# Performance work log

Hardware: AMD Instinct MI355X
Metric: run time of the kernel (lower is better)

The kernel has to match this reference:

```python
import jax, jax.numpy as jnp
import numpy as np

N = 20000      # total nodes (batched graph)
E = 320000     # total edges
G = 200        # number of graphs in batch
F_IN = 128     # node_feat_dim
HID = 128      # hidden_dim
H = 4          # num_heads
LAT = 128      # latent_dim
O1, O2, O3 = HID // 2, HID, 2 * HID          # per-head out feats of gat1/2/3
D1, D2, D3 = H * O1, H * O2, H * O3          # flattened dims (256, 512, 1024)
NEG_SLOPE = 0.2


def setup_inputs() -> dict:
    key = jax.random.key(0)
    ks = jax.random.split(key, 26)
    nrm = lambda k, shape, fan: jax.random.normal(k, shape, jnp.float32) / np.sqrt(fan)
    inp = {
        "node_feat": jax.random.normal(ks[0], (N, F_IN), jnp.float32),
        "src": jax.random.randint(ks[1], (E,), 0, N),
        "dst": jax.random.randint(ks[2], (E,), 0, N),
        "graph_ids": jnp.sort(jax.random.randint(ks[3], (N,), 0, G)),
        # GAT layer 1
        "W1": nrm(ks[4], (F_IN, D1), F_IN), "al1": nrm(ks[5], (H, O1), O1),
        "ar1": nrm(ks[6], (H, O1), O1), "b1": jnp.zeros((D1,), jnp.float32),
        # GAT layer 2
        "W2": nrm(ks[7], (D1, D2), D1), "al2": nrm(ks[8], (H, O2), O2),
        "ar2": nrm(ks[9], (H, O2), O2), "b2": jnp.zeros((D2,), jnp.float32),
        # GAT layer 3
        "W3": nrm(ks[10], (D2, D3), D2), "al3": nrm(ks[11], (H, O3), O3),
        "ar3": nrm(ks[12], (H, O3), O3), "b3": jnp.zeros((D3,), jnp.float32),
        # gate MLP of GlobalAttentionPooling: Linear(D3,HID)->ReLU->Linear(HID,1)
        "Wg1": nrm(ks[13], (D3, HID), D3), "bg1": jnp.zeros((HID,), jnp.float32),
        "Wg2": nrm(ks[14], (HID, 1), HID), "bg2": jnp.zeros((1,), jnp.float32),
        # latent heads
        "Wmu": nrm(ks[15], (D3, LAT), D3), "bmu": jnp.zeros((LAT,), jnp.float32),
        "Wlv": nrm(ks[16], (D3, LAT), D3), "blv": jnp.zeros((LAT,), jnp.float32),
    }
    return inp


def gat_layer(x, W, al, ar, b, src, dst, out_feat):
    # dgl GATConv: fc -> per-node attn halves -> edge leaky_relu -> segment softmax over dst -> scatter-agg
    feat = (x @ W).reshape(-1, H, out_feat)            # [N,H,O]
    el = jnp.sum(feat * al[None], axis=-1)             # [N,H]
    er = jnp.sum(feat * ar[None], axis=-1)             # [N,H]
    e = jax.nn.leaky_relu(el[src] + er[dst], NEG_SLOPE)  # [E,H]
    emax = jax.ops.segment_max(e, dst, num_segments=N)   # per-dst max (stable softmax)
    ex = jnp.exp(e - emax[dst])                         # [E,H]
    denom = jax.ops.segment_sum(ex, dst, num_segments=N)
    alpha = ex / jnp.maximum(denom[dst], 1e-9)          # [E,H]
    msg = feat[src] * alpha[..., None]                  # [E,H,O]
    rst = jax.ops.segment_sum(msg, dst, num_segments=N)  # [N,H,O] (zero for 0-in-degree)
    return rst.reshape(-1, H * out_feat) + b            # flatten(1) + bias


def reference(node_feat, src, dst, graph_ids,
              W1, al1, ar1, b1, W2, al2, ar2, b2, W3, al3, ar3, b3,
              Wg1, bg1, Wg2, bg2, Wmu, bmu, Wlv, blv):
    h = jax.nn.elu(gat_layer(node_feat, W1, al1, ar1, b1, src, dst, O1))
    h = jax.nn.elu(gat_layer(h, W2, al2, ar2, b2, src, dst, O2))
    h = jax.nn.elu(gat_layer(h, W3, al3, ar3, b3, src, dst, O3))
    # GlobalAttentionPooling: gate MLP -> per-graph softmax over nodes -> weighted sum
    gate = (jax.nn.relu(h @ Wg1 + bg1) @ Wg2 + bg2)[:, 0]          # [N]
    gmax = jax.ops.segment_max(gate, graph_ids, num_segments=G)
    gexp = jnp.exp(gate - gmax[graph_ids])
    gsum = jax.ops.segment_sum(gexp, graph_ids, num_segments=G)
    a = gexp / jnp.maximum(gsum[graph_ids], 1e-9)                  # [N]
    graph_emb = jax.ops.segment_sum(a[:, None] * h, graph_ids, num_segments=G)  # [G,D3]
    return graph_emb @ Wmu + bmu, graph_emb @ Wlv + blv
```

## Files before the change

### kernel.cpp

```cpp
#include <hip/hip_runtime.h>
#include <math.h>

constexpr int N_NODES = 20000;
constexpr int N_EDGES = 320000;
constexpr int N_GRAPH = 200;
constexpr int F_IN    = 128;
constexpr int NH      = 4;
constexpr int O1 = 64,  O2 = 128, O3 = 256;
constexpr int D1 = 256, D2 = 512, D3 = 1024;
constexpr int LAT  = 128;
constexpr int HIDG = 128;
constexpr int KS_HEADS = 8;
constexpr float NEG_SLOPE = 0.2f;

typedef __attribute__((ext_vector_type(8))) short bf16x8;
typedef __attribute__((ext_vector_type(4))) float f32x4;
typedef __attribute__((ext_vector_type(2))) ushort ushortx2;

__device__ inline void bsplit(float x, ushort& h, ushort& l) {
    unsigned u = __float_as_uint(x);
    unsigned rh = (u + 0x7fffu + ((u >> 16) & 1u)) & 0xffff0000u;
    h = (ushort)(rh >> 16);
    float res = x - __uint_as_float(rh);
    unsigned u2 = __float_as_uint(res);
    l = (ushort)((u2 + 0x7fffu + ((u2 >> 16) & 1u)) >> 16);
}
__device__ inline ushort f2bf(float x) {
    unsigned u = __float_as_uint(x);
    return (ushort)((u + 0x7fffu + ((u >> 16) & 1u)) >> 16);
}
__device__ inline float bf2f(ushort u) { return __uint_as_float(((unsigned)u) << 16); }

__global__ void zero_int(int* __restrict__ p, int n) {
    int i = blockIdx.x * blockDim.x + threadIdx.x;
    if (i < n) p[i] = 0;
}

__global__ void count_deg(const int* __restrict__ dst, int* __restrict__ deg) {
    int e = blockIdx.x * blockDim.x + threadIdx.x;
    if (e < N_EDGES) atomicAdd(&deg[dst[e]], 1);
}

constexpr int SCAN_B = 512;
__global__ __launch_bounds__(SCAN_B)
void scan1(const int* __restrict__ deg, int* __restrict__ rowptr, int* __restrict__ bsum) {
    __shared__ int s[SCAN_B];
    int tid = threadIdx.x;
    int i = blockIdx.x * SCAN_B + tid;
    int v = (i < N_NODES) ? deg[i] : 0;
    s[tid] = v;
    __syncthreads();
    for (int off = 1; off < SCAN_B; off <<= 1) {
        int add = (tid >= off) ? s[tid - off] : 0;
        __syncthreads();
        s[tid] += add;
        __syncthreads();
    }
    if (i < N_NODES) rowptr[i] = s[tid] - v;
    if (tid == SCAN_B - 1) bsum[blockIdx.x] = s[tid];
}

__global__ void scan2(const int* __restrict__ bsum, int* __restrict__ boff, int nblk) {
    if (threadIdx.x == 0 && blockIdx.x == 0) {
        int run = 0;
        for (int b = 0; b < nblk; ++b) { boff[b] = run; run += bsum[b]; }
    }
}

__global__ __launch_bounds__(SCAN_B)
void scan3(int* __restrict__ rowptr, const int* __restrict__ boff, int* __restrict__ pos) {
    int i = blockIdx.x * SCAN_B + threadIdx.x;
    if (i < N_NODES) {
        int v = rowptr[i] + boff[blockIdx.x];
        rowptr[i] = v;
        pos[i] = v;
    }
    if (i == 0) rowptr[N_NODES] = N_EDGES;
}

__global__ void fill_csr(const int* __restrict__ src, const int* __restrict__ dst,
                         int* __restrict__ pos, int* __restrict__ csr_src) {
    int e = blockIdx.x * blockDim.x + threadIdx.x;
    if (e >= N_EDGES) return;
    int slot = atomicAdd(&pos[dst[e]], 1);
    csr_src[slot] = src[e];
}

__global__ void gptr_kernel(const int* __restrict__ gid, int* __restrict__ gptr) {
    int g = blockIdx.x * blockDim.x + threadIdx.x;
    if (g > N_GRAPH) return;
    int lo = 0, hi = N_NODES;
    while (lo < hi) { int mid = (lo + hi) >> 1; if (gid[mid] < g) lo = mid + 1; else hi = mid; }
    gptr[g] = lo;
}

__global__ void split_x(const float* __restrict__ X, ushort* __restrict__ S, int M, int K) {
    int i = blockIdx.x * 256 + threadIdx.x;
    int total = (M * K) >> 2;
    if (i >= total) return;
    int e0 = i << 2;
    int m = e0 / K, k = e0 % K;
    float4 v = *(const float4*)&X[(size_t)m * K + k];
    ushort h[4], l[4];
    bsplit(v.x, h[0], l[0]); bsplit(v.y, h[1], l[1]);
    bsplit(v.z, h[2], l[2]); bsplit(v.w, h[3], l[3]);
    uint2 hp, lp;
    hp.x = (unsigned)h[0] | ((unsigned)h[1] << 16);
    hp.y = (unsigned)h[2] | ((unsigned)h[3] << 16);
    lp.x = (unsigned)l[0] | ((unsigned)l[1] << 16);
    lp.y = (unsigned)l[2] | ((unsigned)l[3] << 16);
    *(uint2*)&S[(size_t)m * 2 * K + k] = hp;
    *(uint2*)&S[(size_t)m * 2 * K + K + k] = lp;
}

__global__ __launch_bounds__(256)
void split_wt(const float* __restrict__ W, ushort* __restrict__ Bt, int K, int N) {
    __shared__ float t[32][33];
    int n0 = blockIdx.x * 32, k0 = blockIdx.y * 32;
    int tx = threadIdx.x, ty = threadIdx.y;
    for (int j = 0; j < 32; j += 8)
        t[ty + j][tx] = W[(size_t)(k0 + ty + j) * N + n0 + tx];
    __syncthreads();
    for (int j = 0; j < 32; j += 8) {
        float v = t[tx][ty + j];
        int n = n0 + ty + j, k = k0 + tx;
        ushort h, l;
        bsplit(v, h, l);
        Bt[(size_t)n * 2 * K + k] = h;
        Bt[(size_t)n * 2 * K + K + k] = l;
    }
}

#define GLOAD_LDS16(g, s) \
    __builtin_amdgcn_global_load_lds((const __attribute__((address_space(1))) void*)(g), \
                                     (__attribute__((address_space(3))) void*)(s), 16, 0, 0)

template<bool BIAS, bool RELU, int OMODE>
__global__ __launch_bounds__(256)
void gemm_mfma(const ushort* __restrict__ Asp, const ushort* __restrict__ Bt,
               const float* __restrict__ bias, void* __restrict__ Cout,
               int M, int N, int K, int ntn, int kchunk) {
    __shared__ __align__(16) ushort lds[4 * 128 * 64];
    constexpr int AH = 0, AL = 128 * 64, BH = 2 * 128 * 64, BL = 3 * 128 * 64;

    const int nwg = gridDim.x;
    int bid = blockIdx.x;
    int q = nwg >> 3, r = nwg & 7;
    int xcd = bid & 7, local = bid >> 3;
    int wg = (xcd < r) ? (xcd * (q + 1) + local) : (r * (q + 1) + (xcd - r) * q + local);
    const int tm = wg / ntn, tn = wg % ntn;

    const int tid = threadIdx.x;
    const int w = tid >> 6, l = tid & 63;
    const int wr = w >> 1, wc = w & 1;
    const size_t sA = 2 * (size_t)K;

    const int ld8 = l >> 3;
    const int stg_col = ((l & 7) ^ ld8) << 3;
    const int r15 = l & 15, kq = l >> 4;
    const int swz = (l & 7) << 4;

    const int k_begin = blockIdx.y * kchunk;
    const int k_end = (k_begin + kchunk < K) ? (k_begin + kchunk) : K;

    f32x4 acc[4][4];
    #pragma unroll
    for (int m = 0; m < 4; ++m)
        #pragma unroll
        for (int n = 0; n < 4; ++n)
            acc[m][n] = 0.f;

    for (int k0 = k_begin; k0 < k_end; k0 += 64) {
        #pragma unroll
        for (int i = 0; i < 4; ++i) {
            int r0 = w * 32 + i * 8;
            int garow = tm * 128 + r0 + ld8;
            if (garow > M - 1) garow = M - 1;
            const ushort* gaH = Asp + (size_t)garow * sA + k0 + stg_col;
            GLOAD_LDS16(gaH, &lds[AH + r0 * 64]);
            GLOAD_LDS16(gaH + K, &lds[AL + r0 * 64]);
            int gbrow = tn * 128 + r0 + ld8;
            const ushort* gbH = Bt + (size_t)gbrow * sA + k0 + stg_col;
            GLOAD_LDS16(gbH, &lds[BH + r0 * 64]);
            GLOAD_LDS16(gbH + K, &lds[BL + r0 * 64]);
        }
        asm volatile("s_waitcnt vmcnt(0)");
        __syncthreads();

        #pragma unroll
        for (int ks = 0; ks < 2; ++ks) {
            const int kbyte = (ks * 64 + kq * 16) ^ swz;
            bf16x8 ah[4], bh[4], xl[4];
            #pragma unroll
            for (int m = 0; m < 4; ++m) {
                int row = wr * 64 + m * 16 + r15;
                ah[m] = *(const bf16x8*)((const char*)&lds[AH] + row * 128 + kbyte);
            }
            #pragma unroll
            for (int n = 0; n < 4; ++n) {
                int row = wc * 64 + n * 16 + r15;
                bh[n] = *(const bf16x8*)((const char*)&lds[BH] + row * 128 + kbyte);
            }
            #pragma unroll
            for (int m = 0; m < 4; ++m)
                #pragma unroll
                for (int n = 0; n < 4; ++n)
                    acc[m][n] = __builtin_amdgcn_mfma_f32_16x16x32_bf16(ah[m], bh[n], acc[m][n], 0, 0, 0);
            #pragma unroll
            for (int m = 0; m < 4; ++m) {
                int row = wr * 64 + m * 16 + r15;
                xl[m] = *(const bf16x8*)((const char*)&lds[AL] + row * 128 + kbyte);
            }
            #pragma unroll
            for (int m = 0; m < 4; ++m)
                #pragma unroll
                for (int n = 0; n < 4; ++n)
                    acc[m][n] = __builtin_amdgcn_mfma_f32_16x16x32_bf16(xl[m], bh[n], acc[m][n], 0, 0, 0);
            #pragma unroll
            for (int n = 0; n < 4; ++n) {
                int row = wc * 64 + n * 16 + r15;
                xl[n] = *(const bf16x8*)((const char*)&lds[BL] + row * 128 + kbyte);
            }
            #pragma unroll
            for (int m = 0; m < 4; ++m)
                #pragma unroll
                for (int n = 0; n < 4; ++n)
                    acc[m][n] = __builtin_amdgcn_mfma_f32_16x16x32_bf16(ah[m], xl[n], acc[m][n], 0, 0, 0);
        }
        __syncthreads();
    }

    #pragma unroll
    for (int m = 0; m < 4; ++m) {
        #pragma unroll
        for (int n = 0; n < 4; ++n) {
            #pragma unroll
            for (int j = 0; j < 4; ++j) {
                int row = tm * 128 + wr * 64 + m * 16 + kq * 4 + j;
                int col = tn * 128 + wc * 64 + n * 16 + r15;
                if (row < M) {
                    float v = acc[m][n][j];
                    if (BIAS) v += bias[col];
                    if (RELU) v = fmaxf(v, 0.f);
                    if (OMODE == 1)
                        ((ushort*)Cout)[(size_t)row * N + col] = f2bf(v);
                    else if (OMODE == 2)
                        ((float*)Cout)[(size_t)blockIdx.y * M * N + (size_t)row * N + col] = v;
                    else
                        ((float*)Cout)[(size_t)row * N + col] = v;
                }
            }
        }
    }
}

__global__ __launch_bounds__(256)
void attn_lr_b(const ushort* __restrict__ feat, const float* __restrict__ al,
               const float* __restrict__ ar, float* __restrict__ el,
               float* __restrict__ er, int O) {
    int n = blockIdx.x;
    int h = threadIdx.x >> 6;
    int lane = threadIdx.x & 63;
    const ushort* fr = feat + (size_t)n * (NH * O) + h * O;
    const float* alr = al + h * O;
    const float* arr = ar + h * O;
    float sl = 0.f, sr = 0.f;
    for (int o = lane * 2; o < O; o += 128) {
        ushortx2 u = *(const ushortx2*)(fr + o);
        float f0 = bf2f(u[0]), f1 = bf2f(u[1]);
        float2 a2 = *(const float2*)(alr + o);
        float2 r2 = *(const float2*)(arr + o);
        sl += f0 * a2.x + f1 * a2.y;
        sr += f0 * r2.x + f1 * r2.y;
    }
    #pragma unroll
    for (int off = 32; off; off >>= 1) {
        sl += __shfl_down(sl, off);
        sr += __shfl_down(sr, off);
    }
    if (lane == 0) {
        el[n * NH + h] = sl;
        er[n * NH + h] = sr;
    }
}

__global__ __launch_bounds__(64)
void attn_softmax(const float* __restrict__ el, const float* __restrict__ er,
                  const int* __restrict__ rowptr, const int* __restrict__ csr_src,
                  float* __restrict__ csrE, float* __restrict__ rden) {
    int d = blockIdx.x;
    int lane = threadIdx.x;
    int base = __builtin_amdgcn_readfirstlane(rowptr[d]);
    int end  = __builtin_amdgcn_readfirstlane(rowptr[d + 1]);
    float4 erd = *(const float4*)(er + d * NH);

    float mx[NH] = {-INFINITY, -INFINITY, -INFINITY, -INFINITY};
    for (int s = base + lane; s < end; s += 64) {
        int sn = csr_src[s];
        float4 elv = *(const float4*)(el + sn * NH);
        float e0 = elv.x + erd.x, e1 = elv.y + erd.y;
        float e2 = elv.z + erd.z, e3 = elv.w + erd.w;
        e0 = (e0 >= 0.f) ? e0 : NEG_SLOPE * e0;
        e1 = (e1 >= 0.f) ? e1 : NEG_SLOPE * e1;
        e2 = (e2 >= 0.f) ? e2 : NEG_SLOPE * e2;
        e3 = (e3 >= 0.f) ? e3 : NEG_SLOPE * e3;
        csrE[(size_t)0 * N_EDGES + s] = e0;
        csrE[(size_t)1 * N_EDGES + s] = e1;
        csrE[(size_t)2 * N_EDGES + s] = e2;
        csrE[(size_t)3 * N_EDGES + s] = e3;
        mx[0] = fmaxf(mx[0], e0); mx[1] = fmaxf(mx[1], e1);
        mx[2] = fmaxf(mx[2], e2); mx[3] = fmaxf(mx[3], e3);
    }
    #pragma unroll
    for (int h = 0; h < NH; ++h)
        #pragma unroll
        for (int off = 32; off; off >>= 1)
            mx[h] = fmaxf(mx[h], __shfl_xor(mx[h], off));

    float sm[NH] = {0.f, 0.f, 0.f, 0.f};
    for (int s = base + lane; s < end; s += 64) {
        #pragma unroll
        for (int h = 0; h < NH; ++h) {
            float ex = expf(csrE[(size_t)h * N_EDGES + s] - mx[h]);
            csrE[(size_t)h * N_EDGES + s] = ex;
            sm[h] += ex;
        }
    }
    #pragma unroll
    for (int h = 0; h < NH; ++h)
        #pragma unroll
        for (int off = 32; off; off >>= 1)
            sm[h] += __shfl_xor(sm[h], off);

    if (lane == 0) {
        #pragma unroll
        for (int h = 0; h < NH; ++h)
            rden[d * NH + h] = 1.f / fmaxf(sm[h], 1e-9f);
    }
}

template<int OSHIFT, int NCH, int D>
__global__ __launch_bounds__(64)
void aggregate_x(const ushort* __restrict__ feat, const float* __restrict__ csrE,
                 const float* __restrict__ rden, const int* __restrict__ rowptr,
                 const int* __restrict__ csr_src, const float* __restrict__ bias,
                 ushort* __restrict__ Ssp) {
    int bid = blockIdx.x;
    int chunk = bid % NCH;
    int d = bid / NCH;
    int t = threadIdx.x;
    int base = __builtin_amdgcn_readfirstlane(rowptr[d]);
    int end  = __builtin_amdgcn_readfirstlane(rowptr[d + 1]);
    const int col0 = chunk * 128 + t * 2;
    const int h = col0 >> OSHIFT;
    const float* eh = csrE + (size_t)h * N_EDGES;
    const ushort* fcol = feat + col0;

    float acc0 = 0.f, acc1 = 0.f;

    int s = base;
    for (; s < end && (s & 3); ++s) {
        int sn = csr_src[s];
        float a = eh[s];
        ushortx2 u = *(const ushortx2*)(fcol + (size_t)sn * D);
        acc0 += bf2f(u[0]) * a; acc1 += bf2f(u[1]) * a;
    }
    for (; s + 7 < end; s += 8) {
        int4 sa = *(const int4*)(csr_src + s);
        int4 sb = *(const int4*)(csr_src + s + 4);
        float4 aa = *(const float4*)(eh + s);
        float4 ab = *(const float4*)(eh + s + 4);
        ushortx2 u0 = *(const ushortx2*)(fcol + (size_t)sa.x * D);
        ushortx2 u1 = *(const ushortx2*)(fcol + (size_t)sa.y * D);
        ushortx2 u2 = *(const ushortx2*)(fcol + (size_t)sa.z * D);
        ushortx2 u3 = *(const ushortx2*)(fcol + (size_t)sa.w * D);
        ushortx2 u4 = *(const ushortx2*)(fcol + (size_t)sb.x * D);
        ushortx2 u5 = *(const ushortx2*)(fcol + (size_t)sb.y * D);
        ushortx2 u6 = *(const ushortx2*)(fcol + (size_t)sb.z * D);
        ushortx2 u7 = *(const ushortx2*)(fcol + (size_t)sb.w * D);
        acc0 += bf2f(u0[0]) * aa.x; acc1 += bf2f(u0[1]) * aa.x;
        acc0 += bf2f(u1[0]) * aa.y; acc1 += bf2f(u1[1]) * aa.y;
        acc0 += bf2f(u2[0]) * aa.z; acc1 += bf2f(u2[1]) * aa.z;
        acc0 += bf2f(u3[0]) * aa.w; acc1 += bf2f(u3[1]) * aa.w;
        acc0 += bf2f(u4[0]) * ab.x; acc1 += bf2f(u4[1]) * ab.x;
        acc0 += bf2f(u5[0]) * ab.y; acc1 += bf2f(u5[1]) * ab.y;
        acc0 += bf2f(u6[0]) * ab.z; acc1 += bf2f(u6[1]) * ab.z;
        acc0 += bf2f(u7[0]) * ab.w; acc1 += bf2f(u7[1]) * ab.w;
    }
    if (s + 3 < end) {
        int4 sn = *(const int4*)(csr_src + s);
        float4 av = *(const float4*)(eh + s);
        ushortx2 u0 = *(const ushortx2*)(fcol + (size_t)sn.x * D);
        ushortx2 u1 = *(const ushortx2*)(fcol + (size_t)sn.y * D);
        ushortx2 u2 = *(const ushortx2*)(fcol + (size_t)sn.z * D);
        ushortx2 u3 = *(const ushortx2*)(fcol + (size_t)sn.w * D);
        acc0 += bf2f(u0[0]) * av.x; acc1 += bf2f(u0[1]) * av.x;
        acc0 += bf2f(u1[0]) * av.y; acc1 += bf2f(u1[1]) * av.y;
        acc0 += bf2f(u2[0]) * av.z; acc1 += bf2f(u2[1]) * av.z;
        acc0 += bf2f(u3[0]) * av.w; acc1 += bf2f(u3[1]) * av.w;
        s += 4;
    }
    for (; s < end; ++s) {
        int sn = csr_src[s];
        float a = eh[s];
        ushortx2 u = *(const ushortx2*)(fcol + (size_t)sn * D);
        acc0 += bf2f(u[0]) * a; acc1 += bf2f(u[1]) * a;
    }

    float rd = rden[d * NH + h];
    float v0 = acc0 * rd + bias[col0];
    float v1 = acc1 * rd + bias[col0 + 1];
    v0 = (v0 > 0.f) ? v0 : expm1f(v0);
    v1 = (v1 > 0.f) ? v1 : expm1f(v1);
    ushort h0, l0, h1, l1;
    bsplit(v0, h0, l0);
    bsplit(v1, h1, l1);
    ushort* hrow = Ssp + (size_t)d * 2 * D;
    ushortx2 hp, lp;
    hp[0] = h0; hp[1] = h1;
    lp[0] = l0; lp[1] = l1;
    *(ushortx2*)(hrow + col0) = hp;
    *(ushortx2*)(hrow + D + col0) = lp;
}

__global__ __launch_bounds__(128)
void gate_reduce(const float* __restrict__ part, const float* __restrict__ bg1,
                 const float* __restrict__ Wg2, const float* __restrict__ bg2,
                 float* __restrict__ gate) {
    int n = blockIdx.x;
    int t = threadIdx.x;
    constexpr size_t CH = (size_t)N_NODES * HIDG;
    size_t idx = (size_t)n * HIDG + t;
    float v = part[idx] + part[CH + idx] + part[2 * CH + idx] + part[3 * CH + idx] + bg1[t];
    v = fmaxf(v, 0.f) * Wg2[t];
    __shared__ float red[128];
    red[t] = v;
    __syncthreads();
    for (int s = 64; s; s >>= 1) {
        if (t < s) red[t] += red[t + s];
        __syncthreads();
    }
    if (t == 0) gate[n] = red[0] + bg2[0];
}

__global__ __launch_bounds__(64)
void gate_stats(const float* __restrict__ gate, const int* __restrict__ gptr,
                float* __restrict__ anorm) {
    int g = blockIdx.x;
    int lane = threadIdx.x;
    int s = __builtin_amdgcn_readfirstlane(gptr[g]);
    int e = __builtin_amdgcn_readfirstlane(gptr[g + 1]);
    float m = -INFINITY;
    for (int n = s + lane; n < e; n += 64) m = fmaxf(m, gate[n]);
    #pragma unroll
    for (int off = 32; off; off >>= 1) m = fmaxf(m, __shfl_xor(m, off));
    float sum = 0.f;
    for (int n = s + lane; n < e; n += 64) sum += expf(gate[n] - m);
    #pragma unroll
    for (int off = 32; off; off >>= 1) sum += __shfl_xor(sum, off);
    float inv = 1.f / fmaxf(sum, 1e-9f);
    for (int n = s + lane; n < e; n += 64) anorm[n] = expf(gate[n] - m) * inv;
}

__global__ __launch_bounds__(64)
void pool_gather(const ushort* __restrict__ h3sp, const float* __restrict__ anorm,
                 const int* __restrict__ gptr, float* __restrict__ gemb) {
    int g = blockIdx.y;
    int col = blockIdx.x * 128 + threadIdx.x * 2;
    float acc0 = 0.f, acc1 = 0.f;
    int s = __builtin_amdgcn_readfirstlane(gptr[g]);
    int e = __builtin_amdgcn_readfirstlane(gptr[g + 1]);
    int n = s;
    for (; n + 3 < e; n += 4) {
        const ushort* r0 = h3sp + (size_t)(n + 0) * 2 * D3;
        const ushort* r1 = h3sp + (size_t)(n + 1) * 2 * D3;
        const ushort* r2 = h3sp + (size_t)(n + 2) * 2 * D3;
        const ushort* r3 = h3sp + (size_t)(n + 3) * 2 * D3;
        float a0 = anorm[n], a1 = anorm[n + 1], a2 = anorm[n + 2], a3 = anorm[n + 3];
        ushortx2 h0 = *(const ushortx2*)(r0 + col), l0 = *(const ushortx2*)(r0 + D3 + col);
        ushortx2 h1 = *(const ushortx2*)(r1 + col), l1 = *(const ushortx2*)(r1 + D3 + col);
        ushortx2 h2 = *(const ushortx2*)(r2 + col), l2 = *(const ushortx2*)(r2 + D3 + col);
        ushortx2 h3 = *(const ushortx2*)(r3 + col), l3 = *(const ushortx2*)(r3 + D3 + col);
        acc0 += a0 * (bf2f(h0[0]) + bf2f(l0[0])); acc1 += a0 * (bf2f(h0[1]) + bf2f(l0[1]));
        acc0 += a1 * (bf2f(h1[0]) + bf2f(l1[0])); acc1 += a1 * (bf2f(h1[1]) + bf2f(l1[1]));
        acc0 += a2 * (bf2f(h2[0]) + bf2f(l2[0])); acc1 += a2 * (bf2f(h2[1]) + bf2f(l2[1]));
        acc0 += a3 * (bf2f(h3[0]) + bf2f(l3[0])); acc1 += a3 * (bf2f(h3[1]) + bf2f(l3[1]));
    }
    for (; n < e; ++n) {
        const ushort* r0 = h3sp + (size_t)n * 2 * D3;
        float a0 = anorm[n];
        ushortx2 h0 = *(const ushortx2*)(r0 + col), l0 = *(const ushortx2*)(r0 + D3 + col);
        acc0 += a0 * (bf2f(h0[0]) + bf2f(l0[0]));
        acc1 += a0 * (bf2f(h0[1]) + bf2f(l0[1]));
    }
    gemb[(size_t)g * D3 + col] = acc0;
    gemb[(size_t)g * D3 + col + 1] = acc1;
}

__global__ __launch_bounds__(256)
void heads_partial(const float* __restrict__ gemb, const float* __restrict__ Wmu,
                   const float* __restrict__ Wlv, float* __restrict__ part) {
    int g = blockIdx.x, kc = blockIdx.y;
    int t = threadIdx.x;
    int j = t & 127;
    bool lv = t >= 128;
    __shared__ float e[128];
    if (t < 128) e[t] = gemb[(size_t)g * D3 + kc * 128 + t];
    __syncthreads();
    const float* W = (lv ? Wlv : Wmu) + (size_t)(kc * 128) * LAT + j;
    float s = 0.f;
    #pragma unroll 8
    for (int k = 0; k < 128; ++k) s += e[k] * W[(size_t)k * LAT];
    part[((size_t)kc * N_GRAPH + g) * 256 + t] = s;
}

__global__ __launch_bounds__(256)
void heads_reduce(const float* __restrict__ part, const float* __restrict__ bmu,
                  const float* __restrict__ blv, float* __restrict__ out) {
    int g = blockIdx.x;
    int t = threadIdx.x;
    int j = t & 127;
    bool lv = t >= 128;
    float s = 0.f;
    #pragma unroll
    for (int kc = 0; kc < KS_HEADS; ++kc)
        s += part[((size_t)kc * N_GRAPH + g) * 256 + t];
    s += (lv ? blv : bmu)[j];
    out[(lv ? (size_t)N_GRAPH * LAT : 0) + (size_t)g * LAT + j] = s;
}

extern "C" void kernel_launch(void* const* d_in, const int* in_sizes, int n_in,
                              void* d_out, int out_size, void* d_ws, size_t ws_size,
                              hipStream_t stream) {
    const float* node_feat = (const float*)d_in[0];
    const int*   src = (const int*)d_in[1];
    const int*   dst = (const int*)d_in[2];
    const int*   gid = (const int*)d_in[3];
    const float* W1  = (const float*)d_in[4];
    const float* al1 = (const float*)d_in[5];
    const float* ar1 = (const float*)d_in[6];
    const float* b1  = (const float*)d_in[7];
    const float* W2  = (const float*)d_in[8];
    const float* al2 = (const float*)d_in[9];
    const float* ar2 = (const float*)d_in[10];
    const float* b2  = (const float*)d_in[11];
    const float* W3  = (const float*)d_in[12];
    const float* al3 = (const float*)d_in[13];
    const float* ar3 = (const float*)d_in[14];
    const float* b3  = (const float*)d_in[15];
    const float* Wg1 = (const float*)d_in[16];
    const float* bg1 = (const float*)d_in[17];
    const float* Wg2 = (const float*)d_in[18];
    const float* bg2 = (const float*)d_in[19];
    const float* Wmu = (const float*)d_in[20];
    const float* bmu = (const float*)d_in[21];
    const float* Wlv = (const float*)d_in[22];
    const float* blv = (const float*)d_in[23];
    float* out = (float*)d_out;

    char* wsb = (char*)d_ws;
    float* bufA   = (float*)wsb;
    wsb += (size_t)N_NODES * D3 * 4;
    ushort* Xsp   = (ushort*)wsb;
    wsb += (size_t)N_NODES * 2048 * 2;
    ushort* Bt1   = (ushort*)wsb; wsb += (size_t)D1 * 2 * F_IN * 2;
    ushort* Bt2   = (ushort*)wsb; wsb += (size_t)D2 * 2 * D1 * 2;
    ushort* Bt3   = (ushort*)wsb; wsb += (size_t)D3 * 2 * D2 * 2;
    ushort* Btg   = (ushort*)wsb; wsb += (size_t)HIDG * 2 * D3 * 2;
    float* el     = (float*)wsb;  wsb += (size_t)N_NODES * NH * 4;
    float* er     = (float*)wsb;  wsb += (size_t)N_NODES * NH * 4;
    float* rden   = (float*)wsb;  wsb += (size_t)N_NODES * NH * 4;
    float* csrE   = (float*)wsb;  wsb += (size_t)N_EDGES * NH * 4;
    float* gate   = (float*)wsb;  wsb += (size_t)N_NODES * 4;
    float* anorm  = (float*)wsb;  wsb += (size_t)N_NODES * 4;
    int* deg      = (int*)wsb;    wsb += (size_t)N_NODES * 4;
    int* rowptr   = (int*)wsb;    wsb += (size_t)(N_NODES + 1) * 4;
    int* pos      = (int*)wsb;    wsb += (size_t)N_NODES * 4;
    int* csr_src  = (int*)wsb;    wsb += (size_t)N_EDGES * 4;
    int* bsum     = (int*)wsb;    wsb += 64 * 4;
    int* boff     = (int*)wsb;    wsb += 64 * 4;
    int* gptr     = (int*)wsb;    wsb += (size_t)(N_GRAPH + 1) * 4;
    ushort* featb = (ushort*)bufA;
    float* partial = bufA;
    float* gemb   = bufA + (size_t)4 * N_NODES * HIDG;
    float* hpart  = gemb + (size_t)N_GRAPH * D3;

    constexpr int NBLK = (N_NODES + SCAN_B - 1) / SCAN_B;
    zero_int<<<dim3((N_NODES + 255) / 256), dim3(256), 0, stream>>>(deg, N_NODES);
    count_deg<<<dim3((N_EDGES + 255) / 256), dim3(256), 0, stream>>>(dst, deg);
    scan1<<<dim3(NBLK), dim3(SCAN_B), 0, stream>>>(deg, rowptr, bsum);
    scan2<<<dim3(1), dim3(64), 0, stream>>>(bsum, boff, NBLK);
    scan3<<<dim3(NBLK), dim3(SCAN_B), 0, stream>>>(rowptr, boff, pos);
    fill_csr<<<dim3((N_EDGES + 255) / 256), dim3(256), 0, stream>>>(src, dst, pos, csr_src);
    gptr_kernel<<<dim3(1), dim3(256), 0, stream>>>(gid, gptr);

    split_wt<<<dim3(D1 / 32, F_IN / 32), dim3(32, 8), 0, stream>>>(W1, Bt1, F_IN, D1);
    split_wt<<<dim3(D2 / 32, D1 / 32),   dim3(32, 8), 0, stream>>>(W2, Bt2, D1, D2);
    split_wt<<<dim3(D3 / 32, D2 / 32),   dim3(32, 8), 0, stream>>>(W3, Bt3, D2, D3);
    split_wt<<<dim3(HIDG / 32, D3 / 32), dim3(32, 8), 0, stream>>>(Wg1, Btg, D3, HIDG);

    split_x<<<dim3((N_NODES * F_IN / 4 + 255) / 256), dim3(256), 0, stream>>>(node_feat, Xsp, N_NODES, F_IN);

    gemm_mfma<false, false, 1><<<dim3(157 * 2), dim3(256), 0, stream>>>(Xsp, Bt1, nullptr, featb, N_NODES, D1, F_IN, 2, F_IN);
    attn_lr_b<<<dim3(N_NODES), dim3(256), 0, stream>>>(featb, al1, ar1, el, er, O1);
    attn_softmax<<<dim3(N_NODES), dim3(64), 0, stream>>>(el, er, rowptr, csr_src, csrE, rden);
    aggregate_x<6, 2, D1><<<dim3(N_NODES * 2), dim3(64), 0, stream>>>(featb, csrE, rden, rowptr, csr_src, b1, Xsp);

    gemm_mfma<false, false, 1><<<dim3(157 * 4), dim3(256), 0, stream>>>(Xsp, Bt2, nullptr, featb, N_NODES, D2, D1, 4, D1);
    attn_lr_b<<<dim3(N_NODES), dim3(256), 0, stream>>>(featb, al2, ar2, el, er, O2);
    attn_softmax<<<dim3(N_NODES), dim3(64), 0, stream>>>(el, er, rowptr, csr_src, csrE, rden);
    aggregate_x<7, 4, D2><<<dim3(N_NODES * 4), dim3(64), 0, stream>>>(featb, csrE, rden, rowptr, csr_src, b2, Xsp);

    gemm_mfma<false, false, 1><<<dim3(157 * 8), dim3(256), 0, stream>>>(Xsp, Bt3, nullptr, featb, N_NODES, D3, D2, 8, D2);
    attn_lr_b<<<dim3(N_NODES), dim3(256), 0, stream>>>(featb, al3, ar3, el, er, O3);
    attn_softmax<<<dim3(N_NODES), dim3(64), 0, stream>>>(el, er, rowptr, csr_src, csrE, rden);
    aggregate_x<8, 8, D3><<<dim3(N_NODES * 8), dim3(64), 0, stream>>>(featb, csrE, rden, rowptr, csr_src, b3, Xsp);

    gemm_mfma<false, false, 2><<<dim3(157, 4), dim3(256), 0, stream>>>(Xsp, Btg, nullptr, partial, N_NODES, HIDG, D3, 1, D3 / 4);
    gate_reduce<<<dim3(N_NODES), dim3(128), 0, stream>>>(partial, bg1, Wg2, bg2, gate);
    gate_stats<<<dim3(N_GRAPH), dim3(64), 0, stream>>>(gate, gptr, anorm);
    pool_gather<<<dim3(D3 / 128, N_GRAPH), dim3(64), 0, stream>>>(Xsp, anorm, gptr, gemb);
    heads_partial<<<dim3(N_GRAPH, KS_HEADS), dim3(256), 0, stream>>>(gemb, Wmu, Wlv, hpart);
    heads_reduce<<<dim3(N_GRAPH), dim3(256), 0, stream>>>(hpart, bmu, blv, out);
}
```

Before: 459.7 us.

## Fuse attention logit projection into GEMM epilogue with atomic accumulation

Computes per-node el/er attention halves directly from the fp32 GEMM accumulators in the epilogue, using 16-lane shuffle reductions and atomicAdd into per-head slots. This removes the separate attn_lr_b kernel per layer and its full re-read of the bf16 feature matrix. In exchange it adds a zeroing kernel before each layer and float atomics, which make summation order nondeterministic.

```diff
diff --git a/kernel.cpp b/kernel.cpp
--- a/kernel.cpp
+++ b/kernel.cpp
@@ -135,11 +135,13 @@
     __builtin_amdgcn_global_load_lds((const __attribute__((address_space(1))) void*)(g), \
                                      (__attribute__((address_space(3))) void*)(s), 16, 0, 0)
 
-template<bool BIAS, bool RELU, int OMODE>
+template<bool BIAS, bool RELU, int OMODE, int OSHIFT>
 __global__ __launch_bounds__(256)
 void gemm_mfma(const ushort* __restrict__ Asp, const ushort* __restrict__ Bt,
                const float* __restrict__ bias, void* __restrict__ Cout,
-               int M, int N, int K, int ntn, int kchunk) {
+               int M, int N, int K, int ntn, int kchunk,
+               const float* __restrict__ al, const float* __restrict__ ar,
+               float* __restrict__ el, float* __restrict__ er) {
     __shared__ __align__(16) ushort lds[4 * 128 * 64];
     constexpr int AH = 0, AL = 128 * 64, BH = 2 * 128 * 64, BL = 3 * 128 * 64;
 
@@ -252,35 +254,40 @@
             }
         }
     }
-}
-
-__global__ __launch_bounds__(256)
-void attn_lr_b(const ushort* __restrict__ feat, const float* __restrict__ al,
-               const float* __restrict__ ar, float* __restrict__ el,
-               float* __restrict__ er, int O) {
-    int n = blockIdx.x;
-    int h = threadIdx.x >> 6;
-    int lane = threadIdx.x & 63;
-    const ushort* fr = feat + (size_t)n * (NH * O) + h * O;
-    const float* alr = al + h * O;
-    const float* arr = ar + h * O;
-    float sl = 0.f, sr = 0.f;
-    for (int o = lane * 2; o < O; o += 128) {
-        ushortx2 u = *(const ushortx2*)(fr + o);
-        float f0 = bf2f(u[0]), f1 = bf2f(u[1]);
-        float2 a2 = *(const float2*)(alr + o);
-        float2 r2 = *(const float2*)(arr + o);
-        sl += f0 * a2.x + f1 * a2.y;
-        sr += f0 * r2.x + f1 * r2.y;
-    }
-    #pragma unroll
-    for (int off = 32; off; off >>= 1) {
-        sl += __shfl_down(sl, off);
-        sr += __shfl_down(sr, off);
-    }
-    if (lane == 0) {
-        el[n * NH + h] = sl;
-        er[n * NH + h] = sr;
+
+    if (OSHIFT > 0) {
+        const int hh = (tn * 128 + wc * 64) >> OSHIFT;
+        float alv[4], arv[4];
+        #pragma unroll
+        for (int n = 0; n < 4; ++n) {
+            int col = tn * 128 + wc * 64 + n * 16 + r15;
+            alv[n] = al[col];
+            arv[n] = ar[col];
+        }
+        #pragma unroll
+        for (int m = 0; m < 4; ++m) {
+            #pragma unroll
+            for (int j = 0; j < 4; ++j) {
+                float sl = 0.f, sr = 0.f;
+                #pragma unroll
+                for (int n = 0; n < 4; ++n) {
+                    sl += acc[m][n][j] * alv[n];
+                    sr += acc[m][n][j] * arv[n];
+                }
+                #pragma unroll
+                for (int off = 1; off < 16; off <<= 1) {
+                    sl += __shfl_xor(sl, off);
+                    sr += __shfl_xor(sr, off);
+                }
+                if (r15 == 0) {
+                    int row = tm * 128 + wr * 64 + m * 16 + kq * 4 + j;
+                    if (row < M) {
+                        atomicAdd(&el[row * NH + hh], sl);
+                        atomicAdd(&er[row * NH + hh], sr);
+                    }
+                }
+            }
+        }
     }
 }
 
@@ -601,22 +608,30 @@
 
     split_x<<<dim3((N_NODES * F_IN / 4 + 255) / 256), dim3(256), 0, stream>>>(node_feat, Xsp, N_NODES, F_IN);
 
-    gemm_mfma<false, false, 1><<<dim3(157 * 2), dim3(256), 0, stream>>>(Xsp, Bt1, nullptr, featb, N_NODES, D1, F_IN, 2, F_IN);
-    attn_lr_b<<<dim3(N_NODES), dim3(256), 0, stream>>>(featb, al1, ar1, el, er, O1);
+    auto zero_eler = [&]() {
+        zero_int<<<dim3((2 * N_NODES * NH + 255) / 256), dim3(256), 0, stream>>>((int*)el, 2 * N_NODES * NH);
+    };
+
+    zero_eler();
+    gemm_mfma<false, false, 1, 6><<<dim3(157 * 2), dim3(256), 0, stream>>>(
+        Xsp, Bt1, nullptr, featb, N_NODES, D1, F_IN, 2, F_IN, al1, ar1, el, er);
     attn_softmax<<<dim3(N_NODES), dim3(64), 0, stream>>>(el, er, rowptr, csr_src, csrE, rden);
     aggregate_x<6, 2, D1><<<dim3(N_NODES * 2), dim3(64), 0, stream>>>(featb, csrE, rden, rowptr, csr_src, b1, Xsp);
 
-    gemm_mfma<false, false, 1><<<dim3(157 * 4), dim3(256), 0, stream>>>(Xsp, Bt2, nullptr, featb, N_NODES, D2, D1, 4, D1);
-    attn_lr_b<<<dim3(N_NODES), dim3(256), 0, stream>>>(featb, al2, ar2, el, er, O2);
+    zero_eler();
+    gemm_mfma<false, false, 1, 7><<<dim3(157 * 4), dim3(256), 0, stream>>>(
+        Xsp, Bt2, nullptr, featb, N_NODES, D2, D1, 4, D1, al2, ar2, el, er);
     attn_softmax<<<dim3(N_NODES), dim3(64), 0, stream>>>(el, er, rowptr, csr_src, csrE, rden);
     aggregate_x<7, 4, D2><<<dim3(N_NODES * 4), dim3(64), 0, stream>>>(featb, csrE, rden, rowptr, csr_src, b2, Xsp);
 
-    gemm_mfma<false, false, 1><<<dim3(157 * 8), dim3(256), 0, stream>>>(Xsp, Bt3, nullptr, featb, N_NODES, D3, D2, 8, D2);
-    attn_lr_b<<<dim3(N_NODES), dim3(256), 0, stream>>>(featb, al3, ar3, el, er, O3);
+    zero_eler();
+    gemm_mfma<false, false, 1, 8><<<dim3(157 * 8), dim3(256), 0, stream>>>(
+        Xsp, Bt3, nullptr, featb, N_NODES, D3, D2, 8, D2, al3, ar3, el, er);
     attn_softmax<<<dim3(N_NODES), dim3(64), 0, stream>>>(el, er, rowptr, csr_src, csrE, rden);
     aggregate_x<8, 8, D3><<<dim3(N_NODES * 8), dim3(64), 0, stream>>>(featb, csrE, rden, rowptr, csr_src, b3, Xsp);
 
-    gemm_mfma<false, false, 2><<<dim3(157, 4), dim3(256), 0, stream>>>(Xsp, Btg, nullptr, partial, N_NODES, HIDG, D3, 1, D3 / 4);
+    gemm_mfma<false, false, 2, 0><<<dim3(157, 4), dim3(256), 0, stream>>>(
+        Xsp, Btg, nullptr, partial, N_NODES, HIDG, D3, 1, D3 / 4, nullptr, nullptr, nullptr, nullptr);
     gate_reduce<<<dim3(N_NODES), dim3(128), 0, stream>>>(partial, bg1, Wg2, bg2, gate);
     gate_stats<<<dim3(N_GRAPH), dim3(64), 0, stream>>>(gate, gptr, anorm);
     pool_gather<<<dim3(D3 / 128, N_GRAPH), dim3(64), 0, stream>>>(Xsp, anorm, gptr, gemb);
```

Result: slower. 514.2 us (+11.9%).
